# Optimization experiments

Hardware: AMD Instinct MI355X
Metric: run time of the kernel (lower is better)

## Reference

```python
import jax, jax.numpy as jnp
import numpy as np

N_NODES = 100000
N_FEATURES = 128
N_FILTERS = 128
N_EDGES = 3200000


def setup_inputs() -> dict:
    key = jax.random.key(0)
    k_x, k_f, k_src, k_dst, k_w = jax.random.split(key, 5)
    x = jax.random.normal(k_x, (N_NODES, N_FEATURES), dtype=jnp.float32)
    filters = jax.random.normal(k_f, (N_FEATURES, N_FILTERS), dtype=jnp.float32)
    edge_src = jax.random.randint(k_src, (N_EDGES,), 0, N_NODES, dtype=jnp.int64)
    edge_dst = jnp.sort(jax.random.randint(k_dst, (N_EDGES,), 0, N_NODES, dtype=jnp.int64))
    edge_weight = jax.random.uniform(k_w, (N_EDGES,), dtype=jnp.float32)
    return {"x": x, "filters": filters, "edge_src": edge_src,
            "edge_dst": edge_dst, "edge_weight": edge_weight}


def reference(x, filters, edge_src, edge_dst, edge_weight):
    # Dense feature transform: XF = x @ filters  -> [N, n_filters]
    XF = jnp.matmul(x, filters)
    # Sparse aggregation: out[d] += w_e * XF[s] for each edge (s, d, w_e)
    # equivalent to torch.sparse.mm(transform, XF) with transform in COO form.
    msgs = XF[edge_src] * edge_weight[:, None]           # [E, n_filters]
    out = jax.ops.segment_sum(msgs, edge_dst, num_segments=N_NODES)
    return out
```

## Files before the change

kernel.cpp:

```cpp
#include <hip/hip_runtime.h>
#include <stdint.h>

#define N_NODES 100000
#define N_FEAT 128
#define N_EDGES 3200000

static __device__ __forceinline__ unsigned int f2bf_u(float f) {
    unsigned int u = __float_as_uint(f);
    u += 0x7FFFu + ((u >> 16) & 1u);
    return u >> 16;
}

typedef __bf16 bf16x8 __attribute__((ext_vector_type(8)));
typedef float f32x4 __attribute__((ext_vector_type(4)));

__global__ __launch_bounds__(256) void k_prep(
        const float* __restrict__ f, unsigned short* __restrict__ fB,
        const int* __restrict__ dst, int* __restrict__ row_ptr) {
    int b = blockIdx.x;
    if (b < 12500) {
        int e = b * 256 + threadIdx.x;
        if (e >= N_EDGES) return;
        int dcur = dst[e];
        if (e == 0) {
            for (int d = 0; d <= dcur; ++d) row_ptr[d] = 0;
        } else {
            int dprev = dst[e - 1];
            for (int d = dprev + 1; d <= dcur; ++d) row_ptr[d] = e;
        }
        if (e == N_EDGES - 1) {
            for (int d = dcur + 1; d <= N_NODES; ++d) row_ptr[d] = N_EDGES;
        }
    } else {
        int i = (b - 12500) * 256 + threadIdx.x;
        if (i >= N_FEAT * N_FEAT) return;
        int n = ((i >> 11) << 4) | ((i >> 3) & 15);
        int k = (((i >> 9) & 3) << 5) | (((i >> 7) & 3) << 3) | (i & 7);
        fB[i] = (unsigned short)f2bf_u(f[k * 128 + n]);
    }
}

__global__ __launch_bounds__(256) void k_xf(
        const float* __restrict__ x,
        const unsigned short* __restrict__ fB,
        unsigned int* __restrict__ xi8,
        float* __restrict__ xscale) {
    __shared__ unsigned short Bbuf[16384];
    int t = threadIdx.x;
    for (int i = 0; i < 8; ++i)
        ((uint4*)Bbuf)[t + i * 256] = ((const uint4*)fB)[t + i * 256];
    __syncthreads();

    int wave = t >> 6, lane = t & 63, m15 = lane & 15, q = lane >> 4;
    int row = blockIdx.x * 64 + wave * 16 + m15;
    int rowc = min(row, N_NODES - 1);

    f32x4 acc[8];
#pragma unroll
    for (int j = 0; j < 8; ++j) acc[j] = f32x4{0.f, 0.f, 0.f, 0.f};

#pragma unroll
    for (int kkidx = 0; kkidx < 4; ++kkidx) {
        const float* ap = x + (size_t)rowc * 128 + kkidx * 32 + q * 8;
        float4 v0 = *(const float4*)ap;
        float4 v1 = *(const float4*)(ap + 4);
        union { bf16x8 v; unsigned short s[8]; } au;
        au.s[0] = (unsigned short)f2bf_u(v0.x);
        au.s[1] = (unsigned short)f2bf_u(v0.y);
        au.s[2] = (unsigned short)f2bf_u(v0.z);
        au.s[3] = (unsigned short)f2bf_u(v0.w);
        au.s[4] = (unsigned short)f2bf_u(v1.x);
        au.s[5] = (unsigned short)f2bf_u(v1.y);
        au.s[6] = (unsigned short)f2bf_u(v1.z);
        au.s[7] = (unsigned short)f2bf_u(v1.w);
#pragma unroll
        for (int j = 0; j < 8; ++j) {
            bf16x8 bfrag = *(const bf16x8*)(Bbuf + (((j * 4 + kkidx) * 64 + lane) * 8));
            acc[j] = __builtin_amdgcn_mfma_f32_16x16x32_bf16(au.v, bfrag, acc[j], 0, 0, 0);
        }
    }

    int rowbase = blockIdx.x * 64 + wave * 16 + q * 4;
#pragma unroll
    for (int r = 0; r < 4; ++r) {
        float mx = 0.f;
#pragma unroll
        for (int j = 0; j < 8; ++j) mx = fmaxf(mx, fabsf(acc[j][r]));
        for (int d = 1; d < 16; d <<= 1) mx = fmaxf(mx, __shfl_xor(mx, d));
        float inv = 127.f / fmaxf(mx, 1e-20f);
        unsigned int u0 = 0, u1 = 0;
#pragma unroll
        for (int bb = 0; bb < 4; ++bb) {
            unsigned int q0 = (unsigned int)(int)(rintf(acc[2 * bb][r] * inv) + 128.f);
            unsigned int q1 = (unsigned int)(int)(rintf(acc[2 * bb + 1][r] * inv) + 128.f);
            u0 |= (q0 & 0xFFu) << (8 * bb);
            u1 |= (q1 & 0xFFu) << (8 * bb);
        }
        int gr = rowbase + r;
        if (gr < N_NODES) {
            xi8[(size_t)gr * 32 + m15] = u0;
            xi8[(size_t)gr * 32 + 16 + m15] = u1;
            if (m15 == 0) xscale[gr] = mx * (1.f / 127.f);
        }
    }
}

__global__ __launch_bounds__(256) void k_aggregate(
        const unsigned int* __restrict__ xi8,
        const float* __restrict__ xscale,
        const int* __restrict__ src,
        const float* __restrict__ w,
        const int* __restrict__ row_ptr,
        float* __restrict__ out) {
    __shared__ uint2 smeta[4][64];
    int wave = threadIdx.x >> 6, lane = threadIdx.x & 63;
    int node = blockIdx.x * 4 + wave;
    if (node >= N_NODES) return;
    int half = lane >> 5, f = lane & 31;
    int start = row_ptr[node], end = row_ptr[node + 1];
    float a0 = 0.f, a1 = 0.f, a2 = 0.f, a3 = 0.f, aw = 0.f;

    for (int e0 = start; e0 < end; e0 += 64) {
        int e = e0 + lane;
        uint2 m = make_uint2(0u, 0u);
        if (e < end) {
            int sv = src[e];
            m.x = (unsigned int)sv;
            m.y = __float_as_uint(w[e] * xscale[sv]);
        }
        smeta[wave][lane] = m;
        int cnt16 = (min(64, end - e0) + 15) & ~15;
        for (int j = 0; j < cnt16; j += 16) {
            unsigned int vv[8]; float wj[8];
#pragma unroll
            for (int u = 0; u < 8; ++u) {
                uint2 mm = smeta[wave][j + u * 2 + half];
                wj[u] = __uint_as_float(mm.y);
                vv[u] = xi8[mm.x * 32 + f];
            }
#pragma unroll
            for (int u = 0; u < 8; ++u) {
                a0 = fmaf(wj[u], (float)( vv[u]         & 0xFFu), a0);
                a1 = fmaf(wj[u], (float)((vv[u] >>  8)  & 0xFFu), a1);
                a2 = fmaf(wj[u], (float)((vv[u] >> 16)  & 0xFFu), a2);
                a3 = fmaf(wj[u], (float)( vv[u] >> 24          ), a3);
                aw += wj[u];
            }
        }
    }
    a0 = fmaf(-128.f, aw, a0);
    a1 = fmaf(-128.f, aw, a1);
    a2 = fmaf(-128.f, aw, a2);
    a3 = fmaf(-128.f, aw, a3);

    a0 += __shfl_xor(a0, 32);
    a1 += __shfl_xor(a1, 32);
    a2 += __shfl_xor(a2, 32);
    a3 += __shfl_xor(a3, 32);
    if (half == 0) {
        float* o = out + (size_t)node * 128 + f;
        o[ 0] = a0;
        o[32] = a1;
        o[64] = a2;
        o[96] = a3;
    }
}

extern "C" void kernel_launch(void* const* d_in, const int* in_sizes, int n_in,
                              void* d_out, int out_size, void* d_ws, size_t ws_size,
                              hipStream_t stream) {
    const float* x        = (const float*)d_in[0];
    const float* filters  = (const float*)d_in[1];
    const int*   edge_src = (const int*)d_in[2];
    const int*   edge_dst = (const int*)d_in[3];
    const float* edge_w   = (const float*)d_in[4];
    float* out = (float*)d_out;

    char* ws = (char*)d_ws;
    unsigned int*   xi8 = (unsigned int*)  (ws);
    float*          xsc = (float*)         (ws + 13ll * 1024 * 1024);
    unsigned short* fB  = (unsigned short*)(ws + 14ll * 1024 * 1024);
    int*            rp  = (int*)           (ws + 15ll * 1024 * 1024);

    hipLaunchKernelGGL(k_prep, dim3(12564), dim3(256), 0, stream,
                       filters, fB, edge_dst, rp);
    hipLaunchKernelGGL(k_xf, dim3(1563), dim3(256), 0, stream,
                       x, fB, xi8, xsc);
    hipLaunchKernelGGL(k_aggregate, dim3(25000), dim3(256), 0, stream,
                       xi8, xsc, edge_src, edge_w, rp, out);
}
```

Before: 196.1 us.

## Fuse prep into GEMM launch and widen gather loads with software pipelining

Merges the row_ptr construction and the filter bf16 conversion into the GEMM kernel, which drops one kernel launch and the fB intermediate. Each GEMM block now converts the filter matrix into shared memory itself, so that conversion is repeated once per block. The aggregate kernel now gives each lane 8 bytes (uint2) of a neighbour's int8 row, so four edges are handled per step with 16 lanes each. It double-buffers the gather loads against the FMAs and reduces across four lane groups, which trades more registers for more memory-level parallelism.

```diff
diff --git a/kernel.cpp b/kernel.cpp
--- a/kernel.cpp
+++ b/kernel.cpp
@@ -4,6 +4,8 @@
 #define N_NODES 100000
 #define N_FEAT 128
 #define N_EDGES 3200000
+#define GEMM_BLOCKS 1563
+#define SCAT_BLOCKS 12500
 
 static __device__ __forceinline__ unsigned int f2bf_u(float f) {
     unsigned int u = __float_as_uint(f);
@@ -14,12 +16,15 @@
 typedef __bf16 bf16x8 __attribute__((ext_vector_type(8)));
 typedef float f32x4 __attribute__((ext_vector_type(4)));
 
-__global__ __launch_bounds__(256) void k_prep(
-        const float* __restrict__ f, unsigned short* __restrict__ fB,
-        const int* __restrict__ dst, int* __restrict__ row_ptr) {
+__global__ __launch_bounds__(256) void k_xf(
+        const float* __restrict__ x, const float* __restrict__ f,
+        const int* __restrict__ dst, int* __restrict__ row_ptr,
+        unsigned int* __restrict__ xi8,
+        float* __restrict__ xscale) {
     int b = blockIdx.x;
-    if (b < 12500) {
-        int e = b * 256 + threadIdx.x;
+    int t = threadIdx.x;
+    if (b >= GEMM_BLOCKS) {
+        int e = (b - GEMM_BLOCKS) * 256 + t;
         if (e >= N_EDGES) return;
         int dcur = dst[e];
         if (e == 0) {
@@ -31,24 +36,17 @@
         if (e == N_EDGES - 1) {
             for (int d = dcur + 1; d <= N_NODES; ++d) row_ptr[d] = N_EDGES;
         }
-    } else {
-        int i = (b - 12500) * 256 + threadIdx.x;
-        if (i >= N_FEAT * N_FEAT) return;
-        int n = ((i >> 11) << 4) | ((i >> 3) & 15);
-        int k = (((i >> 9) & 3) << 5) | (((i >> 7) & 3) << 3) | (i & 7);
-        fB[i] = (unsigned short)f2bf_u(f[k * 128 + n]);
-    }
-}
-
-__global__ __launch_bounds__(256) void k_xf(
-        const float* __restrict__ x,
-        const unsigned short* __restrict__ fB,
-        unsigned int* __restrict__ xi8,
-        float* __restrict__ xscale) {
+        return;
+    }
+
     __shared__ unsigned short Bbuf[16384];
-    int t = threadIdx.x;
-    for (int i = 0; i < 8; ++i)
-        ((uint4*)Bbuf)[t + i * 256] = ((const uint4*)fB)[t + i * 256];
+#pragma unroll 8
+    for (int i = 0; i < 64; ++i) {
+        int idx = t + i * 256;
+        int n = ((idx >> 11) << 4) | ((idx >> 3) & 15);
+        int k = (((idx >> 9) & 3) << 5) | (((idx >> 7) & 3) << 3) | (idx & 7);
+        Bbuf[idx] = (unsigned short)f2bf_u(f[k * 128 + n]);
+    }
     __syncthreads();
 
     int wave = t >> 6, lane = t & 63, m15 = lane & 15, q = lane >> 4;
@@ -116,54 +114,78 @@
     int wave = threadIdx.x >> 6, lane = threadIdx.x & 63;
     int node = blockIdx.x * 4 + wave;
     if (node >= N_NODES) return;
-    int half = lane >> 5, f = lane & 31;
+    int g = lane >> 4, f16 = lane & 15;
+    unsigned int f16o = (unsigned int)(f16 * 8);
     int start = row_ptr[node], end = row_ptr[node + 1];
-    float a0 = 0.f, a1 = 0.f, a2 = 0.f, a3 = 0.f, aw = 0.f;
+    uint2* sm = smeta[wave];
+    const char* xb = (const char*)xi8;
+
+    float a[8] = {0.f, 0.f, 0.f, 0.f, 0.f, 0.f, 0.f, 0.f};
+    float aw = 0.f;
+
+#define LOADJ(J, VV, WW) do {                                              \
+        _Pragma("unroll")                                                  \
+        for (int u = 0; u < 4; ++u) {                                      \
+            uint2 mm = sm[(J) * 16 + u * 4 + g];                           \
+            WW[u] = __uint_as_float(mm.y);                                 \
+            VV[u] = *(const uint2*)(xb + (mm.x + f16o));                   \
+        } } while (0)
+#define FMAJ(VV, WW) do {                                                  \
+        _Pragma("unroll")                                                  \
+        for (int u = 0; u < 4; ++u) {                                      \
+            unsigned int lo = VV[u].x, hi = VV[u].y; float wu = WW[u];     \
+            aw += wu;                                                      \
+            a[0] = fmaf(wu, (float)( lo        & 0xFFu), a[0]);            \
+            a[1] = fmaf(wu, (float)((lo >>  8) & 0xFFu), a[1]);            \
+            a[2] = fmaf(wu, (float)((lo >> 16) & 0xFFu), a[2]);            \
+            a[3] = fmaf(wu, (float)( lo >> 24         ), a[3]);            \
+            a[4] = fmaf(wu, (float)( hi        & 0xFFu), a[4]);            \
+            a[5] = fmaf(wu, (float)((hi >>  8) & 0xFFu), a[5]);            \
+            a[6] = fmaf(wu, (float)((hi >> 16) & 0xFFu), a[6]);            \
+            a[7] = fmaf(wu, (float)( hi >> 24         ), a[7]);            \
+        } } while (0)
 
     for (int e0 = start; e0 < end; e0 += 64) {
         int e = e0 + lane;
         uint2 m = make_uint2(0u, 0u);
         if (e < end) {
             int sv = src[e];
-            m.x = (unsigned int)sv;
+            m.x = (unsigned int)sv << 7;
             m.y = __float_as_uint(w[e] * xscale[sv]);
         }
-        smeta[wave][lane] = m;
-        int cnt16 = (min(64, end - e0) + 15) & ~15;
-        for (int j = 0; j < cnt16; j += 16) {
-            unsigned int vv[8]; float wj[8];
-#pragma unroll
-            for (int u = 0; u < 8; ++u) {
-                uint2 mm = smeta[wave][j + u * 2 + half];
-                wj[u] = __uint_as_float(mm.y);
-                vv[u] = xi8[mm.x * 32 + f];
-            }
-#pragma unroll
-            for (int u = 0; u < 8; ++u) {
-                a0 = fmaf(wj[u], (float)( vv[u]         & 0xFFu), a0);
-                a1 = fmaf(wj[u], (float)((vv[u] >>  8)  & 0xFFu), a1);
-                a2 = fmaf(wj[u], (float)((vv[u] >> 16)  & 0xFFu), a2);
-                a3 = fmaf(wj[u], (float)( vv[u] >> 24          ), a3);
-                aw += wj[u];
-            }
-        }
-    }
-    a0 = fmaf(-128.f, aw, a0);
-    a1 = fmaf(-128.f, aw, a1);
-    a2 = fmaf(-128.f, aw, a2);
-    a3 = fmaf(-128.f, aw, a3);
-
-    a0 += __shfl_xor(a0, 32);
-    a1 += __shfl_xor(a1, 32);
-    a2 += __shfl_xor(a2, 32);
-    a3 += __shfl_xor(a3, 32);
-    if (half == 0) {
-        float* o = out + (size_t)node * 128 + f;
-        o[ 0] = a0;
-        o[32] = a1;
-        o[64] = a2;
-        o[96] = a3;
-    }
+        sm[lane] = m;
+        int nj = (min(64, end - e0) + 15) >> 4;
+        uint2 v0[4], v1[4]; float w0[4], w1[4];
+        LOADJ(0, v0, w0);
+        int j = 0;
+        for (; j + 2 <= nj; j += 2) {
+            LOADJ(j + 1, v1, w1);
+            FMAJ(v0, w0);
+            if (j + 2 < nj) LOADJ(j + 2, v0, w0);
+            FMAJ(v1, w1);
+        }
+        if (j < nj) FMAJ(v0, w0);
+    }
+
+#pragma unroll
+    for (int k = 0; k < 8; ++k) {
+        a[k] += __shfl_xor(a[k], 16);
+        a[k] += __shfl_xor(a[k], 32);
+    }
+    aw += __shfl_xor(aw, 16);
+    aw += __shfl_xor(aw, 32);
+#pragma unroll
+    for (int k = 0; k < 8; ++k) a[k] = fmaf(-128.f, aw, a[k]);
+
+    if (g == 0) {
+        float* o = out + (size_t)node * 128 + f16 * 2;
+        *(float2*)(o)      = make_float2(a[0], a[4]);
+        *(float2*)(o + 32) = make_float2(a[1], a[5]);
+        *(float2*)(o + 64) = make_float2(a[2], a[6]);
+        *(float2*)(o + 96) = make_float2(a[3], a[7]);
+    }
+#undef LOADJ
+#undef FMAJ
 }
 
 extern "C" void kernel_launch(void* const* d_in, const int* in_sizes, int n_in,
@@ -177,15 +199,12 @@
     float* out = (float*)d_out;
 
     char* ws = (char*)d_ws;
-    unsigned int*   xi8 = (unsigned int*)  (ws);
-    float*          xsc = (float*)         (ws + 13ll * 1024 * 1024);
-    unsigned short* fB  = (unsigned short*)(ws + 14ll * 1024 * 1024);
-    int*            rp  = (int*)           (ws + 15ll * 1024 * 1024);
-
-    hipLaunchKernelGGL(k_prep, dim3(12564), dim3(256), 0, stream,
-                       filters, fB, edge_dst, rp);
-    hipLaunchKernelGGL(k_xf, dim3(1563), dim3(256), 0, stream,
-                       x, fB, xi8, xsc);
+    unsigned int* xi8 = (unsigned int*)(ws);
+    float*        xsc = (float*)       (ws + 13ll * 1024 * 1024);
+    int*          rp  = (int*)         (ws + 15ll * 1024 * 1024);
+
+    hipLaunchKernelGGL(k_xf, dim3(GEMM_BLOCKS + SCAT_BLOCKS), dim3(256), 0, stream,
+                       x, filters, edge_dst, rp, xi8, xsc);
     hipLaunchKernelGGL(k_aggregate, dim3(25000), dim3(256), 0, stream,
                        xi8, xsc, edge_src, edge_w, rp, out);
 }
```

Measured after the change: 224.8 us. 1.15x slower.

## Gather int8 rows with 16-byte loads per 8-lane group and software-prefetch

Applied to the files above, without the earlier changes.

Each group of 8 lanes now gathers one full 128-byte int8 row with uint4 loads, giving 8 edges in flight per wave instead of 2 rows of 4-byte loads. The next group's row is prefetched while the current one is accumulated, and partial sums are reduced across the groups with shuffles at the end. The weight sum is accumulated once per edge from the metadata. This trades more shuffle reductions and more accumulator registers for wider, fewer gather transactions.

```diff
diff --git a/kernel.cpp b/kernel.cpp
--- a/kernel.cpp
+++ b/kernel.cpp
@@ -116,53 +116,79 @@
     int wave = threadIdx.x >> 6, lane = threadIdx.x & 63;
     int node = blockIdx.x * 4 + wave;
     if (node >= N_NODES) return;
-    int half = lane >> 5, f = lane & 31;
+    int g8 = lane >> 3, l8 = lane & 7;
+    unsigned int bo = (unsigned int)(l8 * 16);
     int start = row_ptr[node], end = row_ptr[node + 1];
-    float a0 = 0.f, a1 = 0.f, a2 = 0.f, a3 = 0.f, aw = 0.f;
+    uint2* sm = smeta[wave];
+    const char* xb = (const char*)xi8;
+
+    f32x4 acc[4];
+#pragma unroll
+    for (int b = 0; b < 4; ++b) acc[b] = f32x4{0.f, 0.f, 0.f, 0.f};
+    float aw = 0.f;
+
+#define FMAU(QQ, CC) do {                                                    \
+        acc[0][CC] = fmaf(wu_, (float)( (QQ)        & 0xFFu), acc[0][CC]);   \
+        acc[1][CC] = fmaf(wu_, (float)(((QQ) >>  8) & 0xFFu), acc[1][CC]);   \
+        acc[2][CC] = fmaf(wu_, (float)(((QQ) >> 16) & 0xFFu), acc[2][CC]);   \
+        acc[3][CC] = fmaf(wu_, (float)( (QQ) >> 24         ), acc[3][CC]);   \
+    } while (0)
+#define FMAG(V, WUU) do { float wu_ = __uint_as_float(WUU);                  \
+        FMAU((V).x, 0); FMAU((V).y, 1); FMAU((V).z, 2); FMAU((V).w, 3);      \
+    } while (0)
 
     for (int e0 = start; e0 < end; e0 += 64) {
         int e = e0 + lane;
         uint2 m = make_uint2(0u, 0u);
         if (e < end) {
             int sv = src[e];
-            m.x = (unsigned int)sv;
+            m.x = (unsigned int)sv << 7;
             m.y = __float_as_uint(w[e] * xscale[sv]);
         }
-        smeta[wave][lane] = m;
-        int cnt16 = (min(64, end - e0) + 15) & ~15;
-        for (int j = 0; j < cnt16; j += 16) {
-            unsigned int vv[8]; float wj[8];
-#pragma unroll
-            for (int u = 0; u < 8; ++u) {
-                uint2 mm = smeta[wave][j + u * 2 + half];
-                wj[u] = __uint_as_float(mm.y);
-                vv[u] = xi8[mm.x * 32 + f];
-            }
-#pragma unroll
-            for (int u = 0; u < 8; ++u) {
-                a0 = fmaf(wj[u], (float)( vv[u]         & 0xFFu), a0);
-                a1 = fmaf(wj[u], (float)((vv[u] >>  8)  & 0xFFu), a1);
-                a2 = fmaf(wj[u], (float)((vv[u] >> 16)  & 0xFFu), a2);
-                a3 = fmaf(wj[u], (float)( vv[u] >> 24          ), a3);
-                aw += wj[u];
-            }
-        }
-    }
-    a0 = fmaf(-128.f, aw, a0);
-    a1 = fmaf(-128.f, aw, a1);
-    a2 = fmaf(-128.f, aw, a2);
-    a3 = fmaf(-128.f, aw, a3);
-
-    a0 += __shfl_xor(a0, 32);
-    a1 += __shfl_xor(a1, 32);
-    a2 += __shfl_xor(a2, 32);
-    a3 += __shfl_xor(a3, 32);
-    if (half == 0) {
-        float* o = out + (size_t)node * 128 + f;
-        o[ 0] = a0;
-        o[32] = a1;
-        o[64] = a2;
-        o[96] = a3;
+        sm[lane] = m;
+        aw += __uint_as_float(m.y);
+        int ng = (min(64, end - e0) + 7) >> 3;
+        uint2 mm0 = sm[g8];
+        uint4 v0 = *(const uint4*)(xb + (mm0.x + bo));
+        for (int j = 0; j + 1 < ng; ++j) {
+            uint2 mm1 = sm[(j + 1) * 8 + g8];
+            uint4 v1 = *(const uint4*)(xb + (mm1.x + bo));
+            FMAG(v0, mm0.y);
+            mm0 = mm1; v0 = v1;
+        }
+        FMAG(v0, mm0.y);
+    }
+#undef FMAU
+#undef FMAG
+
+#pragma unroll
+    for (int b = 0; b < 4; ++b)
+#pragma unroll
+        for (int cc = 0; cc < 4; ++cc) {
+            float v = acc[b][cc];
+            v += __shfl_xor(v, 8);
+            v += __shfl_xor(v, 16);
+            v += __shfl_xor(v, 32);
+            acc[b][cc] = v;
+        }
+    aw += __shfl_xor(aw, 1);
+    aw += __shfl_xor(aw, 2);
+    aw += __shfl_xor(aw, 4);
+    aw += __shfl_xor(aw, 8);
+    aw += __shfl_xor(aw, 16);
+    aw += __shfl_xor(aw, 32);
+
+    if (g8 == 0) {
+        float* o = out + (size_t)node * 128 + l8 * 4;
+#pragma unroll
+        for (int b = 0; b < 4; ++b) {
+            float4 ov;
+            ov.x = fmaf(-128.f, aw, acc[b][0]);
+            ov.y = fmaf(-128.f, aw, acc[b][1]);
+            ov.z = fmaf(-128.f, aw, acc[b][2]);
+            ov.w = fmaf(-128.f, aw, acc[b][3]);
+            *(float4*)(o + b * 32) = ov;
+        }
     }
 }
 
```

New measurement: 200.9 us. 2.5% more time.
